# Kernel tuning notes

Measured on AMD Instinct MI355X. Metric: run time of the kernel, lower is better.

The kernel has to match this reference:

```python
import jax, jax.numpy as jnp
import numpy as np

MAXDISP = 48
NUM_GROUPS = 40
CONCAT_CH = 12
BN_EPS = 1e-5


def conv3d(x, w):
    # x: [B,C,D,H,W], w: [O,I,3,3,3], stride 1, pad 1
    return jax.lax.conv_general_dilated(
        x, w, window_strides=(1, 1, 1), padding=[(1, 1), (1, 1), (1, 1)],
        dimension_numbers=('NCDHW', 'OIDHW', 'NCDHW'))


def bn_relu(x, gamma, beta, mean, var):
    # inference-style BatchNorm3d followed by ReLU
    inv = gamma * jax.lax.rsqrt(var + BN_EPS)
    sh = (1, -1, 1, 1, 1)
    return jax.nn.relu(x * inv.reshape(sh) + (beta - mean * inv).reshape(sh))


def build_volume(lg, rg, lc, rc):
    # Fused gwc + concat volume: for disparity d, valid region is columns [d:].
    # Columns [:d] are zero (matches the torch new_zeros + sliced writes).
    B, Cg, H, W = lg.shape
    cpg = Cg // NUM_GROUPS
    slices = []
    for d in range(MAXDISP):  # fixed structural loop over disparities
        if d == 0:
            l, r, lcc, rcc = lg, rg, lc, rc
        else:
            l = lg[:, :, :, d:]
            r = rg[:, :, :, :W - d]
            lcc = lc[:, :, :, d:]
            rcc = rc[:, :, :, :W - d]
        corr = (l * r).reshape(B, NUM_GROUPS, cpg, H, W - d).mean(axis=2)
        s = jnp.concatenate([corr, lcc, rcc], axis=1)  # [B, G+2Cc, H, W-d]
        if d > 0:
            s = jnp.pad(s, ((0, 0), (0, 0), (0, 0), (d, 0)))
        slices.append(s)
    return jnp.stack(slices, axis=2)  # [B, G+2Cc, D, H, W]


def setup_inputs() -> dict:
    key = jax.random.key(0)
    ks = jax.random.split(key, 10)
    B, H, W = 4, 64, 128
    Cin = NUM_GROUPS + 2 * CONCAT_CH  # 64
    f32 = jnp.float32
    return {
        'left_gwc': jax.random.normal(ks[0], (B, 320, H, W), f32),
        'right_gwc': jax.random.normal(ks[1], (B, 320, H, W), f32),
        'left_concat': jax.random.normal(ks[2], (B, CONCAT_CH, H, W), f32),
        'right_concat': jax.random.normal(ks[3], (B, CONCAT_CH, H, W), f32),
        'w1': jax.random.normal(ks[4], (32, Cin, 3, 3, 3), f32) * 0.05,
        'g1': jnp.ones((32,), f32),
        'b1': jnp.zeros((32,), f32),
        'm1': jnp.zeros((32,), f32),
        'v1': jnp.ones((32,), f32),
        'w2': jax.random.normal(ks[5], (32, 32, 3, 3, 3), f32) * 0.05,
        'g2': jnp.ones((32,), f32),
        'b2': jnp.zeros((32,), f32),
        'm2': jnp.zeros((32,), f32),
        'v2': jnp.ones((32,), f32),
    }


def reference(left_gwc, right_gwc, left_concat, right_concat,
              w1, g1, b1, m1, v1, w2, g2, b2, m2, v2):
    vol = build_volume(left_gwc, right_gwc, left_concat, right_concat)
    x = bn_relu(conv3d(vol, w1), g1, b1, m1, v1)
    x = bn_relu(conv3d(x, w2), g2, b2, m2, v2)
    return x  # [B, 32, D, H, W]
```

## Files before the change

### kernel.cpp

```cpp
#include <hip/hip_runtime.h>
#include <cstdint>
#include <cstddef>

typedef unsigned short u16;
typedef __bf16 bf16x8 __attribute__((ext_vector_type(8)));
typedef float f32x4 __attribute__((ext_vector_type(4)));

#define MAXDISP 48
#define HH 64
#define WW 128

__device__ __forceinline__ float bf2f(unsigned int x) {
    union { unsigned int i; float f; } c; c.i = x << 16; return c.f;
}
__device__ __forceinline__ float bf2f_hi(unsigned int x) {
    union { unsigned int i; float f; } c; c.i = x & 0xffff0000u; return c.f;
}
__device__ __forceinline__ u16 f2bf(float f) {
    union { float f; unsigned int i; } c; c.f = f;
    unsigned int x = c.i;
    return (u16)((x + 0x7fffu + ((x >> 16) & 1u)) >> 16);
}

__global__ __launch_bounds__(256) void wfrag_kernel(
    const float* __restrict__ w, const float* __restrict__ gam,
    const float* __restrict__ bet, const float* __restrict__ mea,
    const float* __restrict__ var,
    u16* __restrict__ dst, float* __restrict__ bias, int CIN, int KC)
{
    int idx = blockIdx.x * 256 + threadIdx.x;
    int n = 9 * 2 * KC * 512;
    if (idx < n) {
        int j    = idx & 7;
        int lane = (idx >> 3) & 63;
        int t2   = idx >> 9;
        int kc   = t2 % KC;
        int t3   = t2 / KC;
        int nt   = t3 & 1;
        int tap  = t3 >> 1;
        int co   = nt * 16 + (lane & 15);
        int qq   = lane >> 4;
        int kw, c;
        if (CIN == 64) { kw = kc >> 1; c = (kc & 1) * 32 + qq * 8 + j; }
        else           { kw = kc;      c = qq * 8 + j; }
        int kd = tap / 3, kh = tap % 3;
        float inv = gam[co] * rsqrtf(var[co] + 1e-5f);
        dst[idx] = f2bf(w[((size_t)co * CIN + c) * 27 + kd * 9 + kh * 3 + kw] * inv);
    }
    if (blockIdx.x == 0 && threadIdx.x < 32) {
        int co = threadIdx.x;
        float inv = gam[co] * rsqrtf(var[co] + 1e-5f);
        bias[co] = bet[co] - mea[co] * inv;
    }
}

#define RS 334
__global__ __launch_bounds__(256) void vol_build_kernel(
    const float* __restrict__ lg, const float* __restrict__ rg,
    const float* __restrict__ lc, const float* __restrict__ rc,
    u16* __restrict__ vol, int b0)
{
    __shared__ u16 r_s[128 * RS];
    __shared__ u16 o_s[4 * 128 * 68];

    int bi  = blockIdx.x;
    int h   = bi & 63;
    int dh  = (bi >> 6) & 1;
    int bl  = bi >> 7;
    int b   = b0 + bl;
    int tid = threadIdx.x;
    int w    = tid & 127;
    int part = tid >> 7;

    for (int idx = tid; idx < 320 * 32; idx += 256) {
        int c = idx >> 5, w4 = (idx & 31) << 2;
        const float4 v = *(const float4*)(rg + (((size_t)b * 320 + c) * 64 + h) * 128 + w4);
        r_s[(w4 + 0) * RS + c] = f2bf(v.x);
        r_s[(w4 + 1) * RS + c] = f2bf(v.y);
        r_s[(w4 + 2) * RS + c] = f2bf(v.z);
        r_s[(w4 + 3) * RS + c] = f2bf(v.w);
    }
    for (int idx = tid; idx < 12 * 32; idx += 256) {
        int c = idx >> 5, w4 = (idx & 31) << 2;
        const float4 v = *(const float4*)(rc + (((size_t)b * 12 + c) * 64 + h) * 128 + w4);
        r_s[(w4 + 0) * RS + 320 + c] = f2bf(v.x);
        r_s[(w4 + 1) * RS + 320 + c] = f2bf(v.y);
        r_s[(w4 + 2) * RS + 320 + c] = f2bf(v.z);
        r_s[(w4 + 3) * RS + 320 + c] = f2bf(v.w);
    }
    u16 lcv[12];
    if (part == 0) {
#pragma unroll
        for (int k = 0; k < 12; k++)
            lcv[k] = f2bf(lc[(((size_t)b * 12 + k) * 64 + h) * 128 + w]);
    }
    __syncthreads();

    int d0 = dh * 24;
    for (int dc = 0; dc < 24; dc += 4) {
        for (int gb = 0; gb < 5; gb++) {
            int g0 = part * 20 + gb * 4;
            float lv[4][8];
#pragma unroll
            for (int gg = 0; gg < 4; gg++)
#pragma unroll
                for (int j = 0; j < 8; j++)
                    lv[gg][j] = lg[(((size_t)b * 320 + (g0 + gg) * 8 + j) * 64 + h) * 128 + w];
#pragma unroll
            for (int dl = 0; dl < 4; dl++) {
                int d = d0 + dc + dl;
                union { u16 us[4]; uint2 u2; } pk;
                pk.us[0] = pk.us[1] = pk.us[2] = pk.us[3] = 0;
                if (w >= d) {
#pragma unroll
                    for (int gg = 0; gg < 4; gg++) {
                        float s = 0.f;
                        int base = (w - d) * RS + (g0 + gg) * 8;
#pragma unroll
                        for (int jj = 0; jj < 4; jj++) {
                            unsigned int uu = *(const unsigned int*)&r_s[base + jj * 2];
                            s += lv[gg][jj * 2]     * bf2f(uu & 0xffffu);
                            s += lv[gg][jj * 2 + 1] * bf2f_hi(uu);
                        }
                        pk.us[gg] = f2bf(s * 0.125f);
                    }
                }
                *(uint2*)&o_s[(dl * 128 + w) * 68 + g0] = pk.u2;
            }
        }
#pragma unroll
        for (int dl = 0; dl < 4; dl++) {
            int d = d0 + dc + dl;
            union { u16 us[12]; uint2 u2[3]; } z;
            if (part == 0) {
#pragma unroll
                for (int k = 0; k < 12; k++) z.us[k] = (w >= d) ? lcv[k] : (u16)0;
                u16* dst = &o_s[(dl * 128 + w) * 68 + 40];
                *(uint2*)(dst + 0) = z.u2[0];
                *(uint2*)(dst + 4) = z.u2[1];
                *(uint2*)(dst + 8) = z.u2[2];
            } else {
                if (w >= d) {
                    int base = (w - d) * RS + 320;
#pragma unroll
                    for (int k = 0; k < 12; k++) z.us[k] = r_s[base + k];
                } else {
#pragma unroll
                    for (int k = 0; k < 12; k++) z.us[k] = 0;
                }
                u16* dst = &o_s[(dl * 128 + w) * 68 + 52];
                *(uint2*)(dst + 0) = z.u2[0];
                *(uint2*)(dst + 4) = z.u2[1];
                *(uint2*)(dst + 8) = z.u2[2];
            }
        }
        __syncthreads();
#pragma unroll
        for (int i = 0; i < 16; i++) {
            int idx = i * 256 + tid;
            int dl  = idx >> 10;
            int rem = idx & 1023;
            int ww  = rem >> 3, cg = rem & 7;
            const u16* sp = &o_s[(dl * 128 + ww) * 68 + cg * 8];
            uint2 lo = *(const uint2*)sp;
            uint2 hi = *(const uint2*)(sp + 4);
            uint4 ov = { lo.x, lo.y, hi.x, hi.y };
            int d = d0 + dc + dl;
            *(uint4*)(vol + ((((size_t)bl * 48 + d) * 64 + h) * 128 + ww) * 64 + cg * 8) = ov;
        }
        __syncthreads();
    }
}

__global__ __launch_bounds__(256) void conv1_mfma_kernel(
    const u16* __restrict__ vol, const u16* __restrict__ wf,
    const float* __restrict__ bias, u16* __restrict__ x1)
{
    __shared__ u16 a_s[1170 * 8];

    int bi = blockIdx.x;
    int h  = bi & 63;
    int t1 = bi >> 6;
    int d  = t1 % 48;
    int bl = t1 / 48;
    int tid  = threadIdx.x;
    int lane = tid & 63, wid = tid >> 6;
    int lm = lane & 15, q = lane >> 4;

    f32x4 acc[2][2];
#pragma unroll
    for (int i = 0; i < 2; i++)
#pragma unroll
        for (int j = 0; j < 2; j++) acc[i][j] = { 0.f, 0.f, 0.f, 0.f };

    for (int kd = 0; kd < 3; kd++) {
        int dd = d + kd - 1;
        if (dd < 0 || dd >= 48) continue;
        for (int kh = 0; kh < 3; kh++) {
            int hh = h + kh - 1;
            if (hh < 0 || hh >= 64) continue;
            int tap = kd * 3 + kh;

            __syncthreads();
            const u16* src = vol + (((size_t)bl * 48 + dd) * 64 + hh) * 8192;
#pragma unroll
            for (int i = 0; i < 4; i++) {
                int idx = i * 256 + tid;
                int wp = (idx >> 3) + 1, cg = idx & 7;
                uint4 v = *(const uint4*)(src + idx * 8);
                *(uint4*)&a_s[(wp * 9 + cg) * 8] = v;
            }
            if (tid < 16) {
                uint4 z = { 0, 0, 0, 0 };
                int wp = (tid >> 3) ? 129 : 0;
                *(uint4*)&a_s[(wp * 9 + (tid & 7)) * 8] = z;
            }
            __syncthreads();

            bf16x8 bfr[2][6];
#pragma unroll
            for (int nt = 0; nt < 2; nt++)
#pragma unroll
                for (int kc = 0; kc < 6; kc++)
                    bfr[nt][kc] = *(const bf16x8*)(wf + (((size_t)tap * 2 + nt) * 6 + kc) * 512 + lane * 8);

#pragma unroll
            for (int kc = 0; kc < 6; kc++) {
                int kw = kc >> 1;
                int cg = (kc & 1) * 4 + q;
#pragma unroll
                for (int mt = 0; mt < 2; mt++) {
                    int wp = (wid * 2 + mt) * 16 + lm + kw;
                    bf16x8 afr = *(const bf16x8*)&a_s[(wp * 9 + cg) * 8];
                    acc[mt][0] = __builtin_amdgcn_mfma_f32_16x16x32_bf16(afr, bfr[0][kc], acc[mt][0], 0, 0, 0);
                    acc[mt][1] = __builtin_amdgcn_mfma_f32_16x16x32_bf16(afr, bfr[1][kc], acc[mt][1], 0, 0, 0);
                }
            }
        }
    }

    u16* xb = x1 + (((size_t)bl * 48 + d) * 64 + h) * 4096;
#pragma unroll
    for (int mt = 0; mt < 2; mt++)
#pragma unroll
        for (int nt = 0; nt < 2; nt++) {
            int co = nt * 16 + lm;
            float bs = bias[co];
#pragma unroll
            for (int r = 0; r < 4; r++) {
                int w = (wid * 2 + mt) * 16 + q * 4 + r;
                xb[w * 32 + co] = f2bf(fmaxf(acc[mt][nt][r] + bs, 0.f));
            }
        }
}

__global__ __launch_bounds__(256) void conv2_mfma_kernel(
    const u16* __restrict__ x1, const u16* __restrict__ wf,
    const float* __restrict__ bias, float* __restrict__ out, int b0)
{
    __shared__ u16 a_s[650 * 8];

    int bi = blockIdx.x;
    int h  = bi & 63;
    int t1 = bi >> 6;
    int d  = t1 % 48;
    int bl = t1 / 48;
    int tid  = threadIdx.x;
    int lane = tid & 63, wid = tid >> 6;
    int lm = lane & 15, q = lane >> 4;

    f32x4 acc[2][2];
#pragma unroll
    for (int i = 0; i < 2; i++)
#pragma unroll
        for (int j = 0; j < 2; j++) acc[i][j] = { 0.f, 0.f, 0.f, 0.f };

    for (int kd = 0; kd < 3; kd++) {
        int dd = d + kd - 1;
        if (dd < 0 || dd >= 48) continue;
        for (int kh = 0; kh < 3; kh++) {
            int hh = h + kh - 1;
            if (hh < 0 || hh >= 64) continue;
            int tap = kd * 3 + kh;

            __syncthreads();
            const u16* src = x1 + (((size_t)bl * 48 + dd) * 64 + hh) * 4096;
#pragma unroll
            for (int i = 0; i < 2; i++) {
                int idx = i * 256 + tid;
                int wp = (idx >> 2) + 1, cg = idx & 3;
                uint4 v = *(const uint4*)(src + idx * 8);
                *(uint4*)&a_s[(wp * 5 + cg) * 8] = v;
            }
            if (tid < 8) {
                uint4 z = { 0, 0, 0, 0 };
                int wp = (tid >> 2) ? 129 : 0;
                *(uint4*)&a_s[(wp * 5 + (tid & 3)) * 8] = z;
            }
            __syncthreads();

            bf16x8 bfr[2][3];
#pragma unroll
            for (int nt = 0; nt < 2; nt++)
#pragma unroll
                for (int kc = 0; kc < 3; kc++)
                    bfr[nt][kc] = *(const bf16x8*)(wf + (((size_t)tap * 2 + nt) * 3 + kc) * 512 + lane * 8);

#pragma unroll
            for (int kc = 0; kc < 3; kc++) {
                int kw = kc;
#pragma unroll
                for (int mt = 0; mt < 2; mt++) {
                    int wp = (wid * 2 + mt) * 16 + lm + kw;
                    bf16x8 afr = *(const bf16x8*)&a_s[(wp * 5 + q) * 8];
                    acc[mt][0] = __builtin_amdgcn_mfma_f32_16x16x32_bf16(afr, bfr[0][kc], acc[mt][0], 0, 0, 0);
                    acc[mt][1] = __builtin_amdgcn_mfma_f32_16x16x32_bf16(afr, bfr[1][kc], acc[mt][1], 0, 0, 0);
                }
            }
        }
    }

#pragma unroll
    for (int mt = 0; mt < 2; mt++)
#pragma unroll
        for (int nt = 0; nt < 2; nt++) {
            int co = nt * 16 + lm;
            float bs = bias[co];
            float4 o;
            o.x = fmaxf(acc[mt][nt][0] + bs, 0.f);
            o.y = fmaxf(acc[mt][nt][1] + bs, 0.f);
            o.z = fmaxf(acc[mt][nt][2] + bs, 0.f);
            o.w = fmaxf(acc[mt][nt][3] + bs, 0.f);
            int wbase = (wid * 2 + mt) * 16 + q * 4;
            *(float4*)(out + ((((size_t)(b0 + bl) * 32 + co) * 48 + d) * 64 + h) * 128 + wbase) = o;
        }
}

extern "C" void kernel_launch(void* const* d_in, const int* in_sizes, int n_in,
                              void* d_out, int out_size, void* d_ws, size_t ws_size,
                              hipStream_t stream)
{
    const float* lg = (const float*)d_in[0];
    const float* rg = (const float*)d_in[1];
    const float* lc = (const float*)d_in[2];
    const float* rc = (const float*)d_in[3];
    const float* w1 = (const float*)d_in[4];
    const float* g1 = (const float*)d_in[5];
    const float* b1 = (const float*)d_in[6];
    const float* m1 = (const float*)d_in[7];
    const float* v1 = (const float*)d_in[8];
    const float* w2 = (const float*)d_in[9];
    const float* g2 = (const float*)d_in[10];
    const float* b2 = (const float*)d_in[11];
    const float* m2 = (const float*)d_in[12];
    const float* v2 = (const float*)d_in[13];
    (void)in_sizes; (void)n_in; (void)out_size; (void)ws_size;

    char* ws = (char*)d_ws;
    u16*   wf1   = (u16*)ws;
    u16*   wf2   = (u16*)(ws + 110592);
    float* bias1 = (float*)(ws + 165888);
    float* bias2 = (float*)(ws + 166016);
    u16*   x1    = (u16*)(ws + 166144);

    wfrag_kernel<<<216, 256, 0, stream>>>(w1, g1, b1, m1, v1, wf1, bias1, 64, 6);
    wfrag_kernel<<<108, 256, 0, stream>>>(w2, g2, b2, m2, v2, wf2, bias2, 32, 3);

    for (int r = 0; r < 2; r++) {
        u16* vol = (u16*)d_out + (size_t)r * 50331648;
        vol_build_kernel<<<256, 256, 0, stream>>>(lg, rg, lc, rc, vol, 2 * r);
        conv1_mfma_kernel<<<6144, 256, 0, stream>>>(vol, wf1, bias1, x1);
        conv2_mfma_kernel<<<6144, 256, 0, stream>>>(x1, wf2, bias2, (float*)d_out, 2 * r);
    }
}
```

Measured before the change: 800.3 us.

## Tile four depth slices per block and double-buffer LDS rows in 3D convs

Each conv block now computes four consecutive depth outputs, so every loaded (dd,hh) input row is staged into LDS once and reused by up to three depth outputs instead of being reloaded per output. The row loads are software-pipelined: the next row is fetched into registers while MFMAs run on the current LDS buffer, with two LDS buffers and one barrier per step. Weight fragments are now read from global per MFMA group inside the loop rather than held in registers, and the accumulator count grows fourfold, which raises register pressure (launch bounds set to 3 blocks). The grid shrinks by a factor of four.

Result: slower. 1.136 ms (+42.0%).

```diff
diff --git a/kernel.cpp b/kernel.cpp
--- a/kernel.cpp
+++ b/kernel.cpp
@@ -172,168 +172,233 @@
     }
 }
 
-__global__ __launch_bounds__(256) void conv1_mfma_kernel(
+__global__ __launch_bounds__(256, 3) void conv1_mfma_kernel(
     const u16* __restrict__ vol, const u16* __restrict__ wf,
     const float* __restrict__ bias, u16* __restrict__ x1)
 {
-    __shared__ u16 a_s[1170 * 8];
+    __shared__ u16 a_s[2][1170 * 8];
 
     int bi = blockIdx.x;
     int h  = bi & 63;
     int t1 = bi >> 6;
-    int d  = t1 % 48;
-    int bl = t1 / 48;
+    int dt = t1 % 12;
+    int bl = t1 / 12;
+    int d0 = dt * 4;
     int tid  = threadIdx.x;
     int lane = tid & 63, wid = tid >> 6;
     int lm = lane & 15, q = lane >> 4;
 
-    f32x4 acc[2][2];
-#pragma unroll
-    for (int i = 0; i < 2; i++)
-#pragma unroll
-        for (int j = 0; j < 2; j++) acc[i][j] = { 0.f, 0.f, 0.f, 0.f };
-
-    for (int kd = 0; kd < 3; kd++) {
-        int dd = d + kd - 1;
-        if (dd < 0 || dd >= 48) continue;
-        for (int kh = 0; kh < 3; kh++) {
-            int hh = h + kh - 1;
-            if (hh < 0 || hh >= 64) continue;
-            int tap = kd * 3 + kh;
-
-            __syncthreads();
-            const u16* src = vol + (((size_t)bl * 48 + dd) * 64 + hh) * 8192;
-#pragma unroll
-            for (int i = 0; i < 4; i++) {
-                int idx = i * 256 + tid;
-                int wp = (idx >> 3) + 1, cg = idx & 7;
-                uint4 v = *(const uint4*)(src + idx * 8);
-                *(uint4*)&a_s[(wp * 9 + cg) * 8] = v;
-            }
-            if (tid < 16) {
-                uint4 z = { 0, 0, 0, 0 };
-                int wp = (tid >> 3) ? 129 : 0;
-                *(uint4*)&a_s[(wp * 9 + (tid & 7)) * 8] = z;
-            }
-            __syncthreads();
-
-            bf16x8 bfr[2][6];
-#pragma unroll
-            for (int nt = 0; nt < 2; nt++)
-#pragma unroll
-                for (int kc = 0; kc < 6; kc++)
-                    bfr[nt][kc] = *(const bf16x8*)(wf + (((size_t)tap * 2 + nt) * 6 + kc) * 512 + lane * 8);
-
+    if (tid < 32) {
+        uint4 z = { 0, 0, 0, 0 };
+        int bb = tid >> 4, t = tid & 15;
+        int wp = (t >> 3) ? 129 : 0;
+        *(uint4*)&a_s[bb][(wp * 9 + (t & 7)) * 8] = z;
+    }
+
+    f32x4 acc[4][2][2];
+#pragma unroll
+    for (int i = 0; i < 4; i++)
+#pragma unroll
+        for (int j = 0; j < 2; j++)
+#pragma unroll
+            for (int k = 0; k < 2; k++) acc[i][j][k] = { 0.f, 0.f, 0.f, 0.f };
+
+    int khlo = (h == 0) ? 1 : 0;
+    int khhi = (h == 63) ? 1 : 2;
+    int ddlo = (d0 > 0) ? d0 - 1 : 0;
+    int ddhi = (d0 + 4 < 48) ? d0 + 4 : 47;
+
+    uint4 st[4];
+    {
+        const u16* src = vol + (((size_t)bl * 48 + ddlo) * 64 + (h + khlo - 1)) * 8192;
+#pragma unroll
+        for (int i = 0; i < 4; i++) st[i] = *(const uint4*)(src + ((i * 256 + tid) * 8));
+#pragma unroll
+        for (int i = 0; i < 4; i++) {
+            int idx = i * 256 + tid;
+            *(uint4*)&a_s[0][(((idx >> 3) + 1) * 9 + (idx & 7)) * 8] = st[i];
+        }
+    }
+    __syncthreads();
+
+    int par = 0;
+    for (int kh = khlo; kh <= khhi; kh++) {
+        for (int dd = ddlo; dd <= ddhi; dd++) {
+            int dd2 = dd + 1, kh2 = kh;
+            if (dd2 > ddhi) { dd2 = ddlo; kh2 = kh + 1; }
+            bool have_next = (kh2 <= khhi);
+            if (have_next) {
+                const u16* src = vol + (((size_t)bl * 48 + dd2) * 64 + (h + kh2 - 1)) * 8192;
+#pragma unroll
+                for (int i = 0; i < 4; i++) st[i] = *(const uint4*)(src + ((i * 256 + tid) * 8));
+            }
+
+            const u16* asrc = a_s[par];
 #pragma unroll
             for (int kc = 0; kc < 6; kc++) {
                 int kw = kc >> 1;
                 int cg = (kc & 1) * 4 + q;
-#pragma unroll
-                for (int mt = 0; mt < 2; mt++) {
-                    int wp = (wid * 2 + mt) * 16 + lm + kw;
-                    bf16x8 afr = *(const bf16x8*)&a_s[(wp * 9 + cg) * 8];
-                    acc[mt][0] = __builtin_amdgcn_mfma_f32_16x16x32_bf16(afr, bfr[0][kc], acc[mt][0], 0, 0, 0);
-                    acc[mt][1] = __builtin_amdgcn_mfma_f32_16x16x32_bf16(afr, bfr[1][kc], acc[mt][1], 0, 0, 0);
-                }
-            }
-        }
-    }
-
-    u16* xb = x1 + (((size_t)bl * 48 + d) * 64 + h) * 4096;
-#pragma unroll
-    for (int mt = 0; mt < 2; mt++)
-#pragma unroll
-        for (int nt = 0; nt < 2; nt++) {
-            int co = nt * 16 + lm;
-            float bs = bias[co];
-#pragma unroll
-            for (int r = 0; r < 4; r++) {
-                int w = (wid * 2 + mt) * 16 + q * 4 + r;
-                xb[w * 32 + co] = f2bf(fmaxf(acc[mt][nt][r] + bs, 0.f));
-            }
-        }
-}
-
-__global__ __launch_bounds__(256) void conv2_mfma_kernel(
+                bf16x8 afr0 = *(const bf16x8*)&asrc[((((wid * 2 + 0) * 16 + lm + kw) * 9) + cg) * 8];
+                bf16x8 afr1 = *(const bf16x8*)&asrc[((((wid * 2 + 1) * 16 + lm + kw) * 9) + cg) * 8];
+#pragma unroll
+                for (int dl = 0; dl < 4; dl++) {
+                    int kd = dd - d0 - dl + 1;
+                    if (kd >= 0 && kd <= 2) {
+                        int tap = kd * 3 + kh;
+                        const u16* wb = wf + (((size_t)tap * 2) * 6 + kc) * 512 + lane * 8;
+                        bf16x8 b0 = *(const bf16x8*)wb;
+                        bf16x8 b1 = *(const bf16x8*)(wb + 6 * 512);
+                        acc[dl][0][0] = __builtin_amdgcn_mfma_f32_16x16x32_bf16(afr0, b0, acc[dl][0][0], 0, 0, 0);
+                        acc[dl][1][0] = __builtin_amdgcn_mfma_f32_16x16x32_bf16(afr1, b0, acc[dl][1][0], 0, 0, 0);
+                        acc[dl][0][1] = __builtin_amdgcn_mfma_f32_16x16x32_bf16(afr0, b1, acc[dl][0][1], 0, 0, 0);
+                        acc[dl][1][1] = __builtin_amdgcn_mfma_f32_16x16x32_bf16(afr1, b1, acc[dl][1][1], 0, 0, 0);
+                    }
+                }
+            }
+
+            if (have_next) {
+#pragma unroll
+                for (int i = 0; i < 4; i++) {
+                    int idx = i * 256 + tid;
+                    *(uint4*)&a_s[par ^ 1][(((idx >> 3) + 1) * 9 + (idx & 7)) * 8] = st[i];
+                }
+            }
+            __syncthreads();
+            par ^= 1;
+        }
+    }
+
+#pragma unroll
+    for (int dl = 0; dl < 4; dl++) {
+        u16* xb = x1 + (((size_t)bl * 48 + (d0 + dl)) * 64 + h) * 4096;
+#pragma unroll
+        for (int mt = 0; mt < 2; mt++)
+#pragma unroll
+            for (int nt = 0; nt < 2; nt++) {
+                int co = nt * 16 + lm;
+                float bs = bias[co];
+#pragma unroll
+                for (int r = 0; r < 4; r++) {
+                    int w = (wid * 2 + mt) * 16 + q * 4 + r;
+                    xb[w * 32 + co] = f2bf(fmaxf(acc[dl][mt][nt][r] + bs, 0.f));
+                }
+            }
+    }
+}
+
+__global__ __launch_bounds__(256, 3) void conv2_mfma_kernel(
     const u16* __restrict__ x1, const u16* __restrict__ wf,
     const float* __restrict__ bias, float* __restrict__ out, int b0)
 {
-    __shared__ u16 a_s[650 * 8];
+    __shared__ u16 a_s[2][650 * 8];
 
     int bi = blockIdx.x;
     int h  = bi & 63;
     int t1 = bi >> 6;
-    int d  = t1 % 48;
-    int bl = t1 / 48;
+    int dt = t1 % 12;
+    int bl = t1 / 12;
+    int d0 = dt * 4;
     int tid  = threadIdx.x;
     int lane = tid & 63, wid = tid >> 6;
     int lm = lane & 15, q = lane >> 4;
 
-    f32x4 acc[2][2];
-#pragma unroll
-    for (int i = 0; i < 2; i++)
-#pragma unroll
-        for (int j = 0; j < 2; j++) acc[i][j] = { 0.f, 0.f, 0.f, 0.f };
-
-    for (int kd = 0; kd < 3; kd++) {
-        int dd = d + kd - 1;
-        if (dd < 0 || dd >= 48) continue;
-        for (int kh = 0; kh < 3; kh++) {
-            int hh = h + kh - 1;
-            if (hh < 0 || hh >= 64) continue;
-            int tap = kd * 3 + kh;
-
-            __syncthreads();
-            const u16* src = x1 + (((size_t)bl * 48 + dd) * 64 + hh) * 4096;
-#pragma unroll
-            for (int i = 0; i < 2; i++) {
-                int idx = i * 256 + tid;
-                int wp = (idx >> 2) + 1, cg = idx & 3;
-                uint4 v = *(const uint4*)(src + idx * 8);
-                *(uint4*)&a_s[(wp * 5 + cg) * 8] = v;
-            }
-            if (tid < 8) {
-                uint4 z = { 0, 0, 0, 0 };
-                int wp = (tid >> 2) ? 129 : 0;
-                *(uint4*)&a_s[(wp * 5 + (tid & 3)) * 8] = z;
-            }
-            __syncthreads();
-
-            bf16x8 bfr[2][3];
-#pragma unroll
-            for (int nt = 0; nt < 2; nt++)
-#pragma unroll
-                for (int kc = 0; kc < 3; kc++)
-                    bfr[nt][kc] = *(const bf16x8*)(wf + (((size_t)tap * 2 + nt) * 3 + kc) * 512 + lane * 8);
-
+    if (tid < 16) {
+        uint4 z = { 0, 0, 0, 0 };
+        int bb = tid >> 3, t = tid & 7;
+        int wp = (t >> 2) ? 129 : 0;
+        *(uint4*)&a_s[bb][(wp * 5 + (t & 3)) * 8] = z;
+    }
+
+    f32x4 acc[4][2][2];
+#pragma unroll
+    for (int i = 0; i < 4; i++)
+#pragma unroll
+        for (int j = 0; j < 2; j++)
+#pragma unroll
+            for (int k = 0; k < 2; k++) acc[i][j][k] = { 0.f, 0.f, 0.f, 0.f };
+
+    int khlo = (h == 0) ? 1 : 0;
+    int khhi = (h == 63) ? 1 : 2;
+    int ddlo = (d0 > 0) ? d0 - 1 : 0;
+    int ddhi = (d0 + 4 < 48) ? d0 + 4 : 47;
+
+    uint4 st[2];
+    {
+        const u16* src = x1 + (((size_t)bl * 48 + ddlo) * 64 + (h + khlo - 1)) * 4096;
+#pragma unroll
+        for (int i = 0; i < 2; i++) st[i] = *(const uint4*)(src + ((i * 256 + tid) * 8));
+#pragma unroll
+        for (int i = 0; i < 2; i++) {
+            int idx = i * 256 + tid;
+            *(uint4*)&a_s[0][(((idx >> 2) + 1) * 5 + (idx & 3)) * 8] = st[i];
+        }
+    }
+    __syncthreads();
+
+    int par = 0;
+    for (int kh = khlo; kh <= khhi; kh++) {
+        for (int dd = ddlo; dd <= ddhi; dd++) {
+            int dd2 = dd + 1, kh2 = kh;
+            if (dd2 > ddhi) { dd2 = ddlo; kh2 = kh + 1; }
+            bool have_next = (kh2 <= khhi);
+            if (have_next) {
+                const u16* src = x1 + (((size_t)bl * 48 + dd2) * 64 + (h + kh2 - 1)) * 4096;
+#pragma unroll
+                for (int i = 0; i < 2; i++) st[i] = *(const uint4*)(src + ((i * 256 + tid) * 8));
+            }
+
+            const u16* asrc = a_s[par];
 #pragma unroll
             for (int kc = 0; kc < 3; kc++) {
                 int kw = kc;
-#pragma unroll
-                for (int mt = 0; mt < 2; mt++) {
-                    int wp = (wid * 2 + mt) * 16 + lm + kw;
-                    bf16x8 afr = *(const bf16x8*)&a_s[(wp * 5 + q) * 8];
-                    acc[mt][0] = __builtin_amdgcn_mfma_f32_16x16x32_bf16(afr, bfr[0][kc], acc[mt][0], 0, 0, 0);
-                    acc[mt][1] = __builtin_amdgcn_mfma_f32_16x16x32_bf16(afr, bfr[1][kc], acc[mt][1], 0, 0, 0);
-                }
-            }
-        }
-    }
-
-#pragma unroll
-    for (int mt = 0; mt < 2; mt++)
-#pragma unroll
-        for (int nt = 0; nt < 2; nt++) {
-            int co = nt * 16 + lm;
-            float bs = bias[co];
-            float4 o;
-            o.x = fmaxf(acc[mt][nt][0] + bs, 0.f);
-            o.y = fmaxf(acc[mt][nt][1] + bs, 0.f);
-            o.z = fmaxf(acc[mt][nt][2] + bs, 0.f);
-            o.w = fmaxf(acc[mt][nt][3] + bs, 0.f);
-            int wbase = (wid * 2 + mt) * 16 + q * 4;
-            *(float4*)(out + ((((size_t)(b0 + bl) * 32 + co) * 48 + d) * 64 + h) * 128 + wbase) = o;
-        }
+                bf16x8 afr0 = *(const bf16x8*)&asrc[((((wid * 2 + 0) * 16 + lm + kw) * 5) + q) * 8];
+                bf16x8 afr1 = *(const bf16x8*)&asrc[((((wid * 2 + 1) * 16 + lm + kw) * 5) + q) * 8];
+#pragma unroll
+                for (int dl = 0; dl < 4; dl++) {
+                    int kd = dd - d0 - dl + 1;
+                    if (kd >= 0 && kd <= 2) {
+                        int tap = kd * 3 + kh;
+                        const u16* wb = wf + (((size_t)tap * 2) * 3 + kc) * 512 + lane * 8;
+                        bf16x8 b0 = *(const bf16x8*)wb;
+                        bf16x8 b1 = *(const bf16x8*)(wb + 3 * 512);
+                        acc[dl][0][0] = __builtin_amdgcn_mfma_f32_16x16x32_bf16(afr0, b0, acc[dl][0][0], 0, 0, 0);
+                        acc[dl][1][0] = __builtin_amdgcn_mfma_f32_16x16x32_bf16(afr1, b0, acc[dl][1][0], 0, 0, 0);
+                        acc[dl][0][1] = __builtin_amdgcn_mfma_f32_16x16x32_bf16(afr0, b1, acc[dl][0][1], 0, 0, 0);
+                        acc[dl][1][1] = __builtin_amdgcn_mfma_f32_16x16x32_bf16(afr1, b1, acc[dl][1][1], 0, 0, 0);
+                    }
+                }
+            }
+
+            if (have_next) {
+#pragma unroll
+                for (int i = 0; i < 2; i++) {
+                    int idx = i * 256 + tid;
+                    *(uint4*)&a_s[par ^ 1][(((idx >> 2) + 1) * 5 + (idx & 3)) * 8] = st[i];
+                }
+            }
+            __syncthreads();
+            par ^= 1;
+        }
+    }
+
+#pragma unroll
+    for (int dl = 0; dl < 4; dl++) {
+        int d = d0 + dl;
+#pragma unroll
+        for (int mt = 0; mt < 2; mt++)
+#pragma unroll
+            for (int nt = 0; nt < 2; nt++) {
+                int co = nt * 16 + lm;
+                float bs = bias[co];
+                float4 o;
+                o.x = fmaxf(acc[dl][mt][nt][0] + bs, 0.f);
+                o.y = fmaxf(acc[dl][mt][nt][1] + bs, 0.f);
+                o.z = fmaxf(acc[dl][mt][nt][2] + bs, 0.f);
+                o.w = fmaxf(acc[dl][mt][nt][3] + bs, 0.f);
+                int wbase = (wid * 2 + mt) * 16 + q * 4;
+                *(float4*)(out + ((((size_t)(b0 + bl) * 32 + co) * 48 + d) * 64 + h) * 128 + wbase) = o;
+            }
+    }
 }
 
 extern "C" void kernel_launch(void* const* d_in, const int* in_sizes, int n_in,
@@ -369,7 +434,7 @@
     for (int r = 0; r < 2; r++) {
         u16* vol = (u16*)d_out + (size_t)r * 50331648;
         vol_build_kernel<<<256, 256, 0, stream>>>(lg, rg, lc, rc, vol, 2 * r);
-        conv1_mfma_kernel<<<6144, 256, 0, stream>>>(vol, wf1, bias1, x1);
-        conv2_mfma_kernel<<<6144, 256, 0, stream>>>(x1, wf2, bias2, (float*)d_out, 2 * r);
-    }
-}
+        conv1_mfma_kernel<<<1536, 256, 0, stream>>>(vol, wf1, bias1, x1);
+        conv2_mfma_kernel<<<1536, 256, 0, stream>>>(x1, wf2, bias2, (float*)d_out, 2 * r);
+    }
+}
```

## Prefetch next conv tap into registers and swizzle block order for XCD locality

Applied to the files above, without the earlier changes.

Both conv kernels now load the next valid (kd,kh) tap's input row into registers while the current tap's MFMAs run, hiding global load latency behind compute. The zero padding columns are written once at kernel start instead of every tap. Block indices are remapped so consecutive blocks on each of 8 XCDs process contiguous rows, improving L2 reuse of neighbouring rows. The cost is extra registers for staging, which could reduce occupancy.

Result: slower. 1.167 ms (+45.8%).

```diff
diff --git a/kernel.cpp b/kernel.cpp
--- a/kernel.cpp
+++ b/kernel.cpp
@@ -178,7 +178,8 @@
 {
     __shared__ u16 a_s[1170 * 8];
 
-    int bi = blockIdx.x;
+    int p  = blockIdx.x;
+    int bi = (p & 7) * 768 + (p >> 3);
     int h  = bi & 63;
     int t1 = bi >> 6;
     int d  = t1 % 48;
@@ -187,56 +188,78 @@
     int lane = tid & 63, wid = tid >> 6;
     int lm = lane & 15, q = lane >> 4;
 
+    if (tid < 16) {
+        uint4 z = { 0, 0, 0, 0 };
+        int wp = (tid >> 3) ? 129 : 0;
+        *(uint4*)&a_s[(wp * 9 + (tid & 7)) * 8] = z;
+    }
+
     f32x4 acc[2][2];
 #pragma unroll
     for (int i = 0; i < 2; i++)
 #pragma unroll
         for (int j = 0; j < 2; j++) acc[i][j] = { 0.f, 0.f, 0.f, 0.f };
 
-    for (int kd = 0; kd < 3; kd++) {
-        int dd = d + kd - 1;
-        if (dd < 0 || dd >= 48) continue;
-        for (int kh = 0; kh < 3; kh++) {
-            int hh = h + kh - 1;
-            if (hh < 0 || hh >= 64) continue;
-            int tap = kd * 3 + kh;
-
-            __syncthreads();
+    int t = 0;
+    {
+        while (true) {
+            int dd = d + t / 3 - 1, hh = h + (t % 3) - 1;
+            if (dd >= 0 && dd < 48 && hh >= 0 && hh < 64) break;
+            t++;
+        }
+    }
+
+    uint4 st[4];
+    {
+        int dd = d + t / 3 - 1, hh = h + (t % 3) - 1;
+        const u16* src = vol + (((size_t)bl * 48 + dd) * 64 + hh) * 8192;
+#pragma unroll
+        for (int i = 0; i < 4; i++) st[i] = *(const uint4*)(src + (i * 256 + tid) * 8);
+    }
+
+    while (t < 9) {
+        int tn = t + 1;
+        while (tn < 9) {
+            int dd = d + tn / 3 - 1, hh = h + (tn % 3) - 1;
+            if (dd >= 0 && dd < 48 && hh >= 0 && hh < 64) break;
+            tn++;
+        }
+
+        __syncthreads();
+#pragma unroll
+        for (int i = 0; i < 4; i++) {
+            int idx = i * 256 + tid;
+            *(uint4*)&a_s[(((idx >> 3) + 1) * 9 + (idx & 7)) * 8] = st[i];
+        }
+        if (tn < 9) {
+            int dd = d + tn / 3 - 1, hh = h + (tn % 3) - 1;
             const u16* src = vol + (((size_t)bl * 48 + dd) * 64 + hh) * 8192;
 #pragma unroll
-            for (int i = 0; i < 4; i++) {
-                int idx = i * 256 + tid;
-                int wp = (idx >> 3) + 1, cg = idx & 7;
-                uint4 v = *(const uint4*)(src + idx * 8);
-                *(uint4*)&a_s[(wp * 9 + cg) * 8] = v;
+            for (int i = 0; i < 4; i++) st[i] = *(const uint4*)(src + (i * 256 + tid) * 8);
+        }
+        __syncthreads();
+
+        int tap = t;
+        bf16x8 bfr[2][6];
+#pragma unroll
+        for (int nt = 0; nt < 2; nt++)
+#pragma unroll
+            for (int kc = 0; kc < 6; kc++)
+                bfr[nt][kc] = *(const bf16x8*)(wf + (((size_t)tap * 2 + nt) * 6 + kc) * 512 + lane * 8);
+
+#pragma unroll
+        for (int kc = 0; kc < 6; kc++) {
+            int kw = kc >> 1;
+            int cg = (kc & 1) * 4 + q;
+#pragma unroll
+            for (int mt = 0; mt < 2; mt++) {
+                int wp = (wid * 2 + mt) * 16 + lm + kw;
+                bf16x8 afr = *(const bf16x8*)&a_s[(wp * 9 + cg) * 8];
+                acc[mt][0] = __builtin_amdgcn_mfma_f32_16x16x32_bf16(afr, bfr[0][kc], acc[mt][0], 0, 0, 0);
+                acc[mt][1] = __builtin_amdgcn_mfma_f32_16x16x32_bf16(afr, bfr[1][kc], acc[mt][1], 0, 0, 0);
             }
-            if (tid < 16) {
-                uint4 z = { 0, 0, 0, 0 };
-                int wp = (tid >> 3) ? 129 : 0;
-                *(uint4*)&a_s[(wp * 9 + (tid & 7)) * 8] = z;
-            }
-            __syncthreads();
-
-            bf16x8 bfr[2][6];
-#pragma unroll
-            for (int nt = 0; nt < 2; nt++)
-#pragma unroll
-                for (int kc = 0; kc < 6; kc++)
-                    bfr[nt][kc] = *(const bf16x8*)(wf + (((size_t)tap * 2 + nt) * 6 + kc) * 512 + lane * 8);
-
-#pragma unroll
-            for (int kc = 0; kc < 6; kc++) {
-                int kw = kc >> 1;
-                int cg = (kc & 1) * 4 + q;
-#pragma unroll
-                for (int mt = 0; mt < 2; mt++) {
-                    int wp = (wid * 2 + mt) * 16 + lm + kw;
-                    bf16x8 afr = *(const bf16x8*)&a_s[(wp * 9 + cg) * 8];
-                    acc[mt][0] = __builtin_amdgcn_mfma_f32_16x16x32_bf16(afr, bfr[0][kc], acc[mt][0], 0, 0, 0);
-                    acc[mt][1] = __builtin_amdgcn_mfma_f32_16x16x32_bf16(afr, bfr[1][kc], acc[mt][1], 0, 0, 0);
-                }
-            }
-        }
+        }
+        t = tn;
     }
 
     u16* xb = x1 + (((size_t)bl * 48 + d) * 64 + h) * 4096;
@@ -260,7 +283,8 @@
 {
     __shared__ u16 a_s[650 * 8];
 
-    int bi = blockIdx.x;
+    int p  = blockIdx.x;
+    int bi = (p & 7) * 768 + (p >> 3);
     int h  = bi & 63;
     int t1 = bi >> 6;
     int d  = t1 % 48;
@@ -269,55 +293,77 @@
     int lane = tid & 63, wid = tid >> 6;
     int lm = lane & 15, q = lane >> 4;
 
+    if (tid < 8) {
+        uint4 z = { 0, 0, 0, 0 };
+        int wp = (tid >> 2) ? 129 : 0;
+        *(uint4*)&a_s[(wp * 5 + (tid & 3)) * 8] = z;
+    }
+
     f32x4 acc[2][2];
 #pragma unroll
     for (int i = 0; i < 2; i++)
 #pragma unroll
         for (int j = 0; j < 2; j++) acc[i][j] = { 0.f, 0.f, 0.f, 0.f };
 
-    for (int kd = 0; kd < 3; kd++) {
-        int dd = d + kd - 1;
-        if (dd < 0 || dd >= 48) continue;
-        for (int kh = 0; kh < 3; kh++) {
-            int hh = h + kh - 1;
-            if (hh < 0 || hh >= 64) continue;
-            int tap = kd * 3 + kh;
-
-            __syncthreads();
+    int t = 0;
+    {
+        while (true) {
+            int dd = d + t / 3 - 1, hh = h + (t % 3) - 1;
+            if (dd >= 0 && dd < 48 && hh >= 0 && hh < 64) break;
+            t++;
+        }
+    }
+
+    uint4 st[2];
+    {
+        int dd = d + t / 3 - 1, hh = h + (t % 3) - 1;
+        const u16* src = x1 + (((size_t)bl * 48 + dd) * 64 + hh) * 4096;
+#pragma unroll
+        for (int i = 0; i < 2; i++) st[i] = *(const uint4*)(src + (i * 256 + tid) * 8);
+    }
+
+    while (t < 9) {
+        int tn = t + 1;
+        while (tn < 9) {
+            int dd = d + tn / 3 - 1, hh = h + (tn % 3) - 1;
+            if (dd >= 0 && dd < 48 && hh >= 0 && hh < 64) break;
+            tn++;
+        }
+
+        __syncthreads();
+#pragma unroll
+        for (int i = 0; i < 2; i++) {
+            int idx = i * 256 + tid;
+            *(uint4*)&a_s[(((idx >> 2) + 1) * 5 + (idx & 3)) * 8] = st[i];
+        }
+        if (tn < 9) {
+            int dd = d + tn / 3 - 1, hh = h + (tn % 3) - 1;
             const u16* src = x1 + (((size_t)bl * 48 + dd) * 64 + hh) * 4096;
 #pragma unroll
-            for (int i = 0; i < 2; i++) {
-                int idx = i * 256 + tid;
-                int wp = (idx >> 2) + 1, cg = idx & 3;
-                uint4 v = *(const uint4*)(src + idx * 8);
-                *(uint4*)&a_s[(wp * 5 + cg) * 8] = v;
+            for (int i = 0; i < 2; i++) st[i] = *(const uint4*)(src + (i * 256 + tid) * 8);
+        }
+        __syncthreads();
+
+        int tap = t;
+        bf16x8 bfr[2][3];
+#pragma unroll
+        for (int nt = 0; nt < 2; nt++)
+#pragma unroll
+            for (int kc = 0; kc < 3; kc++)
+                bfr[nt][kc] = *(const bf16x8*)(wf + (((size_t)tap * 2 + nt) * 3 + kc) * 512 + lane * 8);
+
+#pragma unroll
+        for (int kc = 0; kc < 3; kc++) {
+            int kw = kc;
+#pragma unroll
+            for (int mt = 0; mt < 2; mt++) {
+                int wp = (wid * 2 + mt) * 16 + lm + kw;
+                bf16x8 afr = *(const bf16x8*)&a_s[(wp * 5 + q) * 8];
+                acc[mt][0] = __builtin_amdgcn_mfma_f32_16x16x32_bf16(afr, bfr[0][kc], acc[mt][0], 0, 0, 0);
+                acc[mt][1] = __builtin_amdgcn_mfma_f32_16x16x32_bf16(afr, bfr[1][kc], acc[mt][1], 0, 0, 0);
             }
-            if (tid < 8) {
-                uint4 z = { 0, 0, 0, 0 };
-                int wp = (tid >> 2) ? 129 : 0;
-                *(uint4*)&a_s[(wp * 5 + (tid & 3)) * 8] = z;
-            }
-            __syncthreads();
-
-            bf16x8 bfr[2][3];
-#pragma unroll
-            for (int nt = 0; nt < 2; nt++)
-#pragma unroll
-                for (int kc = 0; kc < 3; kc++)
-                    bfr[nt][kc] = *(const bf16x8*)(wf + (((size_t)tap * 2 + nt) * 3 + kc) * 512 + lane * 8);
-
-#pragma unroll
-            for (int kc = 0; kc < 3; kc++) {
-                int kw = kc;
-#pragma unroll
-                for (int mt = 0; mt < 2; mt++) {
-                    int wp = (wid * 2 + mt) * 16 + lm + kw;
-                    bf16x8 afr = *(const bf16x8*)&a_s[(wp * 5 + q) * 8];
-                    acc[mt][0] = __builtin_amdgcn_mfma_f32_16x16x32_bf16(afr, bfr[0][kc], acc[mt][0], 0, 0, 0);
-                    acc[mt][1] = __builtin_amdgcn_mfma_f32_16x16x32_bf16(afr, bfr[1][kc], acc[mt][1], 0, 0, 0);
-                }
-            }
-        }
+        }
+        t = tn;
     }
 
 #pragma unroll
```
